# Kernel tuning notes

Hardware: AMD Instinct MI355X
Metric: run time of the kernel (lower is better)

## Reference

```python
import jax, jax.numpy as jnp
import numpy as np

B, S, D, H = 256, 64, 1024, 16
DH = D // H          # 64
BOARD = 8
NREL = 2 * (BOARD - 1) + 1  # 15


def _rel_indices():
    # Relative row/col offsets between all pairs of board squares, shifted to [0, 2*(BOARD-1)]
    coords = np.arange(S)
    row = coords // BOARD
    col = coords % BOARD
    rr = row[:, None] - row[None, :] + (BOARD - 1)  # (S, S)
    rc = col[:, None] - col[None, :] + (BOARD - 1)  # (S, S)
    return jnp.asarray(rr), jnp.asarray(rc)


def setup_inputs() -> dict:
    key = jax.random.key(0)
    ks = jax.random.split(key, 12)
    p = lambda k, sh: jax.random.normal(k, sh, jnp.float32) * 0.02
    return {
        "x": jax.random.normal(ks[0], (B, S, D), jnp.float32),
        "wq": p(ks[1], (D, D)),
        "wk": p(ks[2], (D, D)),
        "wv": p(ks[3], (D, D)),
        "wo": p(ks[4], (D, D)),
        "bo": jnp.zeros((D,), jnp.float32),
        "eq_h": p(ks[5], (NREL, DH)),
        "eq_w": p(ks[6], (NREL, DH)),
        "ek_h": p(ks[7], (NREL, DH)),
        "ek_w": p(ks[8], (NREL, DH)),
        "ev_h": p(ks[9], (NREL, DH)),
        "ev_w": p(ks[10], (NREL, DH)),
    }


def reference(x, wq, wk, wv, wo, bo, eq_h, eq_w, ek_h, ek_w, ev_h, ev_w):
    rr, rc = _rel_indices()
    rel_q = eq_h[rr] + eq_w[rc]  # (S, S, DH)
    rel_k = ek_h[rr] + ek_w[rc]
    rel_v = ev_h[rr] + ev_w[rc]

    def heads(y):
        return y.reshape(B, S, H, DH).transpose(0, 2, 1, 3)  # (B, H, S, DH)

    q = heads(x @ wq.T)
    k = heads(x @ wk.T)
    v = heads(x @ wv.T)

    # (q_i + rq_ij) . (k_j + rk_ij), expanded to avoid the (B,H,S,S,DH) intermediates
    scores = (
        jnp.einsum('bhid,bhjd->bhij', q, k)
        + jnp.einsum('bhid,ijd->bhij', q, rel_k)
        + jnp.einsum('ijd,bhjd->bhij', rel_q, k)
        + jnp.sum(rel_q * rel_k, axis=-1)[None, None]
    )
    attn = jax.nn.softmax(scores / jnp.sqrt(jnp.float32(DH)), axis=-1)  # (B, H, S, S)

    # sum_j attn_ij * (v_j + rv_ij)
    ctx = (
        jnp.einsum('bhij,bhjd->bhid', attn, v)
        + jnp.einsum('bhij,ijd->bhid', attn, rel_v)
    )
    ctx = ctx.transpose(0, 2, 1, 3).reshape(B, S, D)
    return ctx @ wo.T + bo
```

## Files before the change

kernel.cpp:

```cpp
#include <hip/hip_runtime.h>
#include <hip/hip_bf16.h>

typedef __hip_bfloat16 bf16;
typedef __attribute__((ext_vector_type(8))) short short8;
typedef __attribute__((ext_vector_type(8))) unsigned short ushort8;
typedef __attribute__((ext_vector_type(4))) float floatx4;

__device__ __forceinline__ short f2s(float x) {
  bf16 h = __float2bfloat16(x);
  short s;
  __builtin_memcpy(&s, &h, 2);
  return s;
}

__device__ __forceinline__ void gl_lds16(const bf16* g, bf16* l) {
  __builtin_amdgcn_global_load_lds(
      (const __attribute__((address_space(1))) unsigned int*)g,
      (__attribute__((address_space(3))) unsigned int*)l, 16, 0, 0);
}

#define MFMA16(a, b, c) __builtin_amdgcn_mfma_f32_16x16x32_bf16((a), (b), (c), 0, 0, 0)

__device__ __forceinline__ void bar() {
  asm volatile("" ::: "memory");
  __builtin_amdgcn_s_barrier();
  asm volatile("" ::: "memory");
}

#define VMCNT(N) asm volatile("s_waitcnt vmcnt(" #N ")" ::: "memory")

__global__ __launch_bounds__(256) void convert_f32_bf16(
    const float* __restrict__ src, bf16* __restrict__ dst, int n) {
  const int i = (blockIdx.x * 256 + threadIdx.x) * 8;
  if (i + 7 < n) {
    float4 a = *(const float4*)(src + i);
    float4 b = *(const float4*)(src + i + 4);
    short8 r;
    r[0] = f2s(a.x); r[1] = f2s(a.y); r[2] = f2s(a.z); r[3] = f2s(a.w);
    r[4] = f2s(b.x); r[5] = f2s(b.y); r[6] = f2s(b.z); r[7] = f2s(b.w);
    *(short8*)(dst + i) = r;
  }
}

__global__ __launch_bounds__(256) void precompute_tables(
    const float* __restrict__ eqh, const float* __restrict__ eqw,
    const float* __restrict__ ekh, const float* __restrict__ ekw,
    const float* __restrict__ evh, const float* __restrict__ evw,
    bf16* __restrict__ ews, float* __restrict__ S4f)
{
  const int t = threadIdx.x;
  if (t < 96) {
    const int tb = t >> 4, row = t & 15;
    const float* src[6] = {eqh, eqw, ekh, ekw, evh, evw};
    bf16* dst = ews + tb * 1024 + row * 64;
    if (row < 15) {
      const float* s = src[tb] + row * 64;
      #pragma unroll
      for (int d = 0; d < 64; d += 8) {
        float4 a = *(const float4*)(s + d);
        float4 b2 = *(const float4*)(s + d + 4);
        short8 rr;
        rr[0] = f2s(a.x); rr[1] = f2s(a.y); rr[2] = f2s(a.z); rr[3] = f2s(a.w);
        rr[4] = f2s(b2.x); rr[5] = f2s(b2.y); rr[6] = f2s(b2.z); rr[7] = f2s(b2.w);
        *(short8*)(dst + d) = rr;
      }
    } else {
      const short8 z = {0, 0, 0, 0, 0, 0, 0, 0};
      #pragma unroll
      for (int d = 0; d < 64; d += 8) *(short8*)(dst + d) = z;
    }
  }
  if (t < 225) {
    const int r = t / 15, c = t % 15;
    float s = 0.f;
    for (int d = 0; d < 64; ++d)
      s += (eqh[r * 64 + d] + eqw[c * 64 + d]) * (ekh[r * 64 + d] + ekw[c * 64 + d]);
    S4f[t] = s;
  }
}

template <int TAG>
__global__ __launch_bounds__(512, 2) void gemm256(
    const bf16* __restrict__ A,
    const bf16* __restrict__ W0, const bf16* __restrict__ W1, const bf16* __restrict__ W2,
    const float* __restrict__ bias, int hasBias,
    bf16* __restrict__ O0, bf16* __restrict__ O1, bf16* __restrict__ O2,
    float* __restrict__ Ofp, int outF32)
{
  __shared__ bf16 lds[65536];

  const int nx = gridDim.x;
  const int nwg = nx * gridDim.y;
  const int orig = blockIdx.y * nx + blockIdx.x;
  const int id = (orig & 7) * (nwg >> 3) + (orig >> 3);
  const int bx = id % nx;
  const int by = id / nx;

  const int m0 = bx * 256;
  const int which = by >> 2;
  const bf16* W = (which == 0) ? W0 : (which == 1) ? W1 : W2;
  bf16* O = (which == 0) ? O0 : (which == 1) ? O1 : O2;
  const int n0 = (by & 3) * 256;

  const int t = threadIdx.x;
  const int lane = t & 63, w = t >> 6;
  const int wm = w >> 2, wn = w & 3;
  const int quad = lane >> 4, n16 = lane & 15;

  const int srow = (t >> 6) * 16 + ((t & 63) >> 2);
  const int scol = ((t & 3) * 8) ^ (((t >> 5) & 1) << 4);
  const bf16* Abase = A + (m0 + srow) * 1024 + scol;
  const bf16* Bbase = W + (n0 + srow) * 1024 + scol;
  const int wdst = w * 512;

  const int swzq = (quad * 8) ^ ((n16 >> 3) << 4);
  const int aoff = wm * 4096 + n16 * 32 + swzq;
  const int boff = wn * 2048 + n16 * 32 + swzq;

  floatx4 acc[8][4];
  const floatx4 zero4 = {0.f, 0.f, 0.f, 0.f};
  #pragma unroll
  for (int mi = 0; mi < 8; ++mi)
    #pragma unroll
    for (int ni = 0; ni < 4; ++ni) acc[mi][ni] = zero4;

  #pragma unroll
  for (int p = 0; p < 3; ++p) {
    const bf16* ga = Abase + p * 32;
    bf16* la = lds + p * 16384 + wdst;
    gl_lds16(ga, la); gl_lds16(ga + 131072, la + 4096);
    const bf16* gb = Bbase + p * 32;
    bf16* lb = lds + p * 16384 + 8192 + wdst;
    gl_lds16(gb, lb); gl_lds16(gb + 131072, lb + 4096);
  }
  VMCNT(8);
  bar();

#define TILE_STEP(TT, DOSTAGE, WAITSEQ) do {                                   \
    const bf16* bA_ = lds + ((TT) & 3) * 16384;                                \
    const bf16* bB_ = bA_ + 8192;                                              \
    short8 af_[4], bq_[4];                                                     \
    _Pragma("unroll")                                                          \
    for (int mi = 0; mi < 4; ++mi)                                             \
      af_[mi] = *(const short8*)(bA_ + aoff + mi * 512);                       \
    _Pragma("unroll")                                                          \
    for (int ni = 0; ni < 4; ++ni)                                             \
      bq_[ni] = *(const short8*)(bB_ + boff + ni * 512);                       \
    if (DOSTAGE) {                                                             \
      const bf16* g_ = Abase + ((TT) + 3) * 32;                                \
      bf16* l_ = lds + (((TT) + 3) & 3) * 16384 + wdst;                        \
      gl_lds16(g_, l_); gl_lds16(g_ + 131072, l_ + 4096);                      \
    }                                                                          \
    bar();                                                                     \
    __builtin_amdgcn_s_setprio(1);                                             \
    _Pragma("unroll")                                                          \
    for (int mi = 0; mi < 4; ++mi)                                             \
      _Pragma("unroll")                                                        \
      for (int ni = 0; ni < 4; ++ni)                                           \
        acc[mi][ni] = MFMA16(af_[mi], bq_[ni], acc[mi][ni]);                   \
    __builtin_amdgcn_s_setprio(0);                                             \
    _Pragma("unroll")                                                          \
    for (int mi = 0; mi < 4; ++mi)                                             \
      af_[mi] = *(const short8*)(bA_ + aoff + 2048 + mi * 512);                \
    if (DOSTAGE) {                                                             \
      const bf16* g_ = Bbase + ((TT) + 3) * 32;                                \
      bf16* l_ = lds + (((TT) + 3) & 3) * 16384 + 8192 + wdst;                 \
      gl_lds16(g_, l_); gl_lds16(g_ + 131072, l_ + 4096);                      \
    }                                                                          \
    bar();                                                                     \
    __builtin_amdgcn_s_setprio(1);                                             \
    _Pragma("unroll")                                                          \
    for (int mi = 0; mi < 4; ++mi)                                             \
      _Pragma("unroll")                                                        \
      for (int ni = 0; ni < 4; ++ni)                                           \
        acc[mi + 4][ni] = MFMA16(af_[mi], bq_[ni], acc[mi + 4][ni]);           \
    __builtin_amdgcn_s_setprio(0);                                             \
    WAITSEQ;                                                                   \
  } while (0)

  #pragma unroll 1
  for (int tt = 0; tt < 29; ++tt) {
    TILE_STEP(tt, 1, VMCNT(8); bar());
  }
  TILE_STEP(29, 0, VMCNT(4); bar());
  TILE_STEP(30, 0, VMCNT(0); bar());
  TILE_STEP(31, 0, (void)0);
#undef TILE_STEP

  #pragma unroll
  for (int ni = 0; ni < 4; ++ni) {
    const int col = n0 + wn * 64 + ni * 16 + n16;
    const float bv = hasBias ? bias[col] : 0.f;
    #pragma unroll
    for (int mi = 0; mi < 8; ++mi) {
      #pragma unroll
      for (int r = 0; r < 4; ++r) {
        const int row = m0 + wm * 128 + mi * 16 + quad * 4 + r;
        if (outF32) Ofp[row * 1024 + col] = acc[mi][ni][r] + bv;
        else        O[row * 1024 + col] = __float2bfloat16(acc[mi][ni][r] + bv);
      }
    }
  }
}

template <int TAG>
__global__ __launch_bounds__(256) void gemm_bt(
    const bf16* __restrict__ A,
    const void* __restrict__ W0, const void* __restrict__ W1, const void* __restrict__ W2,
    int wBf,
    const float* __restrict__ bias, int hasBias,
    bf16* __restrict__ O0, bf16* __restrict__ O1, bf16* __restrict__ O2,
    float* __restrict__ Ofp, int outF32)
{
  __shared__ bf16 As[128 * 64];
  __shared__ bf16 Bs[128 * 64];

  const int m0 = blockIdx.x * 128;
  const int by = blockIdx.y;
  const int which = by >> 3;
  const void* W = (which == 0) ? W0 : (which == 1) ? W1 : W2;
  bf16* O = (which == 0) ? O0 : (which == 1) ? O1 : O2;
  const int n0 = (by & 7) * 128;

  const int t = threadIdx.x;
  const int lane = t & 63, w = t >> 6;
  const int lrow = lane >> 3, lcol = (lane & 7) * 8;
  const int wm = w >> 1, wn = w & 1;
  const int quad = lane >> 4, n16 = lane & 15;

  const int swzA = ((lrow & 1) << 5) | (((lrow >> 1) & 3) << 3);
  const int gcol = lcol ^ swzA;
  const int swzR = ((n16 & 1) << 5) | (((n16 >> 1) & 3) << 3);

  floatx4 acc[4][4];
  const floatx4 zero4 = {0.f, 0.f, 0.f, 0.f};
  #pragma unroll
  for (int mi = 0; mi < 4; ++mi)
    #pragma unroll
    for (int ni = 0; ni < 4; ++ni) acc[mi][ni] = zero4;

  const int arowb = m0 + w * 32 + lrow;
  const int browb = n0 + w * 32 + lrow;
  bf16* lau = As + w * 2048;
  bf16* lbu = Bs + w * 2048;

  if (wBf) {
    const bf16* Wb = (const bf16*)W;
    for (int k0 = 0; k0 < 1024; k0 += 64) {
      if (k0) __syncthreads();
      const bf16* ga = A + arowb * 1024 + k0 + gcol;
      const bf16* gw = Wb + browb * 1024 + k0 + gcol;
      #pragma unroll
      for (int c = 0; c < 4; ++c) {
        gl_lds16(ga + c * 8192, lau + c * 512);
        gl_lds16(gw + c * 8192, lbu + c * 512);
      }
      __syncthreads();
      #pragma unroll
      for (int ks = 0; ks < 2; ++ks) {
        short8 af[4], bfv[4];
        #pragma unroll
        for (int mi = 0; mi < 4; ++mi)
          af[mi] = *(const short8*)(As + (wm * 64 + mi * 16 + n16) * 64 +
                                    ((ks * 32 + quad * 8) ^ swzR));
        #pragma unroll
        for (int ni = 0; ni < 4; ++ni)
          bfv[ni] = *(const short8*)(Bs + (wn * 64 + ni * 16 + n16) * 64 +
                                     ((ks * 32 + quad * 8) ^ swzR));
        #pragma unroll
        for (int mi = 0; mi < 4; ++mi)
          #pragma unroll
          for (int ni = 0; ni < 4; ++ni)
            acc[mi][ni] = MFMA16(af[mi], bfv[ni], acc[mi][ni]);
      }
    }
  } else {
    const float* Wf = (const float*)W;
    for (int k0 = 0; k0 < 1024; k0 += 64) {
      short8 rb[4];
      #pragma unroll
      for (int c = 0; c < 4; ++c) {
        const float* f = Wf + (browb + c * 8) * 1024 + k0 + gcol;
        float4 a = *(const float4*)f;
        float4 b = *(const float4*)(f + 4);
        short8 r;
        r[0] = f2s(a.x); r[1] = f2s(a.y); r[2] = f2s(a.z); r[3] = f2s(a.w);
        r[4] = f2s(b.x); r[5] = f2s(b.y); r[6] = f2s(b.z); r[7] = f2s(b.w);
        rb[c] = r;
      }
      if (k0) __syncthreads();
      const bf16* ga = A + arowb * 1024 + k0 + gcol;
      #pragma unroll
      for (int c = 0; c < 4; ++c) {
        gl_lds16(ga + c * 8192, lau + c * 512);
        *(short8*)(lbu + lane * 8 + c * 512) = rb[c];
      }
      __syncthreads();
      #pragma unroll
      for (int ks = 0; ks < 2; ++ks) {
        short8 af[4], bfv[4];
        #pragma unroll
        for (int mi = 0; mi < 4; ++mi)
          af[mi] = *(const short8*)(As + (wm * 64 + mi * 16 + n16) * 64 +
                                    ((ks * 32 + quad * 8) ^ swzR));
        #pragma unroll
        for (int ni = 0; ni < 4; ++ni)
          bfv[ni] = *(const short8*)(Bs + (wn * 64 + ni * 16 + n16) * 64 +
                                     ((ks * 32 + quad * 8) ^ swzR));
        #pragma unroll
        for (int mi = 0; mi < 4; ++mi)
          #pragma unroll
          for (int ni = 0; ni < 4; ++ni)
            acc[mi][ni] = MFMA16(af[mi], bfv[ni], acc[mi][ni]);
      }
    }
  }

  #pragma unroll
  for (int ni = 0; ni < 4; ++ni) {
    const int col = n0 + wn * 64 + ni * 16 + n16;
    const float bv = hasBias ? bias[col] : 0.f;
    #pragma unroll
    for (int mi = 0; mi < 4; ++mi) {
      #pragma unroll
      for (int r = 0; r < 4; ++r) {
        const int row = m0 + wm * 64 + mi * 16 + quad * 4 + r;
        if (outF32) Ofp[row * 1024 + col] = acc[mi][ni][r] + bv;
        else        O[row * 1024 + col] = __float2bfloat16(acc[mi][ni][r] + bv);
      }
    }
  }
}

__global__ __launch_bounds__(256, 3) void attn_rel(
    const bf16* __restrict__ Q, const bf16* __restrict__ Km, const bf16* __restrict__ V,
    const bf16* __restrict__ ews, const float* __restrict__ S4f,
    bf16* __restrict__ Ctx)
{
  __shared__ bf16 vT[64][106];
  __shared__ bf16 pa[64][104];
  __shared__ float Ahs[64][16], Aws[64][16];
  __shared__ float Bhs[15][64], Bws[15][64];
  __shared__ float S4s[225];

  const int t = threadIdx.x;
  const int b = blockIdx.x >> 4, h = blockIdx.x & 15;
  const int base = b * 65536 + h * 64;
  const int lane = t & 63, w = t >> 6;
  const int quad = lane >> 4, n16 = lane & 15;

  const bf16* qrow = Q + base + (w * 16 + n16) * 1024 + quad * 8;
  short8 aq0 = *(const short8*)(qrow);
  short8 aq1 = *(const short8*)(qrow + 32);
  short8 bk0[4], bk1[4];
  #pragma unroll
  for (int nj = 0; nj < 4; ++nj) {
    const bf16* krow = Km + base + (nj * 16 + n16) * 1024 + quad * 8;
    bk0[nj] = *(const short8*)(krow);
    bk1[nj] = *(const short8*)(krow + 32);
  }
  short8 ebf[4][2];
  #pragma unroll
  for (int tb = 0; tb < 4; ++tb) {
    const bf16* er = ews + tb * 1024 + n16 * 64 + quad * 8;
    ebf[tb][0] = *(const short8*)(er);
    ebf[tb][1] = *(const short8*)(er + 32);
  }

  {
    const int r = t >> 2, c0 = (t & 3) * 16;
    const bf16* vrow = V + base + r * 1024 + c0;
    int4 v0 = *(const int4*)(vrow);
    int4 v1 = *(const int4*)(vrow + 8);
    const unsigned short* p0 = (const unsigned short*)&v0;
    const unsigned short* p1 = (const unsigned short*)&v1;
    #pragma unroll
    for (int ii = 0; ii < 8; ++ii) {
      *(unsigned short*)&vT[c0 + ii][r] = p0[ii];
      *(unsigned short*)&vT[c0 + 8 + ii][r] = p1[ii];
    }
    if (t < 60) {
      const int r2 = t >> 2, d0 = (t & 3) * 16;
      ushort8 pe0 = *(const ushort8*)(ews + 4096 + r2 * 64 + d0);
      ushort8 pe1 = *(const ushort8*)(ews + 4096 + r2 * 64 + d0 + 8);
      ushort8 pf0 = *(const ushort8*)(ews + 5120 + r2 * 64 + d0);
      ushort8 pf1 = *(const ushort8*)(ews + 5120 + r2 * 64 + d0 + 8);
      #pragma unroll
      for (int ii = 0; ii < 8; ++ii) {
        *(unsigned short*)&vT[d0 + ii][64 + r2] = pe0[ii];
        *(unsigned short*)&vT[d0 + 8 + ii][64 + r2] = pe1[ii];
        *(unsigned short*)&vT[d0 + ii][79 + r2] = pf0[ii];
        *(unsigned short*)&vT[d0 + 8 + ii][79 + r2] = pf1[ii];
      }
    }
    if (t < 64) {
      *(unsigned short*)&vT[t][94] = 0; *(unsigned short*)&vT[t][95] = 0;
      *(unsigned short*)&pa[t][94] = 0; *(unsigned short*)&pa[t][95] = 0;
    }
    if (t < 225) S4s[t] = S4f[t];
  }

  floatx4 cqk[4];
  #pragma unroll
  for (int nj = 0; nj < 4; ++nj) {
    floatx4 c = {0.f, 0.f, 0.f, 0.f};
    c = MFMA16(aq0, bk0[nj], c);
    c = MFMA16(aq1, bk1[nj], c);
    cqk[nj] = c;
  }
  {
    floatx4 cah = {0.f, 0.f, 0.f, 0.f}, caw = cah, cbh = cah, cbw = cah;
    cah = MFMA16(aq0, ebf[2][0], cah); cah = MFMA16(aq1, ebf[2][1], cah);
    caw = MFMA16(aq0, ebf[3][0], caw); caw = MFMA16(aq1, ebf[3][1], caw);
    cbh = MFMA16(bk0[w], ebf[0][0], cbh); cbh = MFMA16(bk1[w], ebf[0][1], cbh);
    cbw = MFMA16(bk0[w], ebf[1][0], cbw); cbw = MFMA16(bk1[w], ebf[1][1], cbw);
    #pragma unroll
    for (int r = 0; r < 4; ++r) {
      const int i = w * 16 + quad * 4 + r;
      Ahs[i][n16] = cah[r];
      Aws[i][n16] = caw[r];
      if (n16 < 15) { Bhs[n16][i] = cbh[r]; Bws[n16][i] = cbw[r]; }
    }
  }
  __syncthreads();

  const int i_base = w * 16 + quad * 4;
  float xv[4][4];
  #pragma unroll
  for (int nj = 0; nj < 4; ++nj) {
    const int j = nj * 16 + n16;
    const int rowj = j >> 3, colj = j & 7;
    #pragma unroll
    for (int r = 0; r < 4; ++r) {
      const int i = i_base + r;
      const int rowi = i >> 3, coli = i & 7;
      const int rr = rowi - rowj + 7, rc = coli - colj + 7;
      xv[r][nj] = (cqk[nj][r] + Ahs[i][rr] + Aws[i][rc] + Bhs[rr][j] + Bws[rc][j]
                   + S4s[rr * 15 + rc]) * 0.125f;
    }
  }
  #pragma unroll
  for (int r = 0; r < 4; ++r) {
    const int i = i_base + r;
    const int rowi = i >> 3, coli = i & 7;
    float mx = fmaxf(fmaxf(xv[r][0], xv[r][1]), fmaxf(xv[r][2], xv[r][3]));
    #pragma unroll
    for (int off = 1; off < 16; off <<= 1) mx = fmaxf(mx, __shfl_xor(mx, off));
    float p[4];
    float sm = 0.f;
    #pragma unroll
    for (int nj = 0; nj < 4; ++nj) { p[nj] = __expf(xv[r][nj] - mx); sm += p[nj]; }
    #pragma unroll
    for (int off = 1; off < 16; off <<= 1) sm += __shfl_xor(sm, off);
    const float inv = 1.0f / sm;
    #pragma unroll
    for (int nj = 0; nj < 4; ++nj) {
      p[nj] *= inv;
      pa[i][nj * 16 + n16] = __float2bfloat16(p[nj]);
    }
    float ph[4];
    #pragma unroll
    for (int nj = 0; nj < 4; ++nj) {
      float v = p[nj];
      v += __shfl_xor(v, 1); v += __shfl_xor(v, 2); v += __shfl_xor(v, 4);
      ph[nj] = v;
    }
    float s4 = p[0] + p[1] + p[2] + p[3];
    float pw = s4 + __shfl_xor(s4, 8);
    if ((n16 & 7) == 0) {
      const int hh = n16 >> 3;
      #pragma unroll
      for (int nj = 0; nj < 4; ++nj) {
        const int g = nj * 2 + hh;
        pa[i][64 + rowi + 7 - g] = __float2bfloat16(ph[nj]);
      }
    } else if (n16 < 8) {
      const int z = n16 - 1;
      pa[i][64 + (z < rowi ? z : z + 8)] = __float2bfloat16(0.f);
    }
    if (n16 < 8) {
      pa[i][79 + coli + 7 - n16] = __float2bfloat16(pw);
    } else {
      const int z = n16 - 8;
      pa[i][79 + (z < coli ? z : z + 8)] = __float2bfloat16(0.f);
    }
  }
  __threadfence_block();

  short8 ap[3];
  #pragma unroll
  for (int ksb = 0; ksb < 3; ++ksb)
    ap[ksb] = *(const short8*)&pa[w * 16 + n16][ksb * 32 + quad * 8];
  #pragma unroll
  for (int nj = 0; nj < 4; ++nj) {
    floatx4 c = {0.f, 0.f, 0.f, 0.f};
    #pragma unroll
    for (int ksb = 0; ksb < 3; ++ksb) {
      short8 bv = *(const short8*)&vT[nj * 16 + n16][ksb * 32 + quad * 8];
      c = MFMA16(ap[ksb], bv, c);
    }
    #pragma unroll
    for (int r = 0; r < 4; ++r) {
      const int i = i_base + r;
      Ctx[base + i * 1024 + nj * 16 + n16] = __float2bfloat16(c[r]);
    }
  }
}

extern "C" void kernel_launch(void* const* d_in, const int* in_sizes, int n_in,
                              void* d_out, int out_size, void* d_ws, size_t ws_size,
                              hipStream_t stream) {
  const float* x   = (const float*)d_in[0];
  const float* wq  = (const float*)d_in[1];
  const float* wk  = (const float*)d_in[2];
  const float* wv  = (const float*)d_in[3];
  const float* wo  = (const float*)d_in[4];
  const float* bo  = (const float*)d_in[5];
  const float* eqh = (const float*)d_in[6];
  const float* eqw = (const float*)d_in[7];
  const float* ekh = (const float*)d_in[8];
  const float* ekw = (const float*)d_in[9];
  const float* evh = (const float*)d_in[10];
  const float* evw = (const float*)d_in[11];
  float* outf = (float*)d_out;

  const size_t hdr = (ws_size - 16384) & ~(size_t)1023;
  bf16* ewsB = (bf16*)((char*)d_ws + hdr);
  float* S4f = (float*)((char*)d_ws + hdr + 12288);
  precompute_tables<<<1, 256, 0, stream>>>(eqh, eqw, ekh, ekw, evh, evw, ewsB, S4f);

  if (ws_size >= (size_t)73 * 1024 * 1024) {
    bf16* qb = (bf16*)d_ws;
    bf16* kb = qb + 16777216;
    bf16* wqb = kb + 16777216;
    bf16* wkb = wqb + 1048576;
    bf16* wvb = wkb + 1048576;
    bf16* wob = wvb + 1048576;
    bf16* xb = (bf16*)d_out;
    bf16* vb = (bf16*)((char*)d_out + 33554432);

    convert_f32_bf16<<<8192, 256, 0, stream>>>(x, xb, 16777216);
    convert_f32_bf16<<<512, 256, 0, stream>>>(wq, wqb, 1048576);
    convert_f32_bf16<<<512, 256, 0, stream>>>(wk, wkb, 1048576);
    convert_f32_bf16<<<512, 256, 0, stream>>>(wv, wvb, 1048576);
    convert_f32_bf16<<<512, 256, 0, stream>>>(wo, wob, 1048576);

    gemm256<0><<<dim3(64, 12), 512, 0, stream>>>(
        xb, wqb, wkb, wvb, nullptr, 0, qb, kb, vb, nullptr, 0);
    attn_rel<<<dim3(4096), 256, 0, stream>>>(qb, kb, vb, ewsB, S4f, qb);
    gemm256<1><<<dim3(64, 4), 512, 0, stream>>>(
        qb, wob, nullptr, nullptr, bo, 1, nullptr, nullptr, nullptr, outf, 1);
  } else {
    bf16* xb0 = (bf16*)((char*)d_out + 16777216);
    bf16* xb1 = (bf16*)((char*)d_out + 50331648);
    bf16* vQ2 = (bf16*)((char*)d_out + 33554432);
    bf16* qb = (bf16*)d_ws;
    bf16* kb = qb + 8388608;
    const int fastW = (ws_size >= (size_t)42 * 1024 * 1024) ? 1 : 0;
    bf16* wqb = kb + 8388608;
    bf16* wkb = wqb + 1048576;
    bf16* wvb = wkb + 1048576;
    bf16* wob = wvb + 1048576;

    convert_f32_bf16<<<4096, 256, 0, stream>>>(x, xb0, 8388608);
    convert_f32_bf16<<<4096, 256, 0, stream>>>(x + 8388608, xb1, 8388608);
    if (fastW) {
      convert_f32_bf16<<<512, 256, 0, stream>>>(wq, wqb, 1048576);
      convert_f32_bf16<<<512, 256, 0, stream>>>(wk, wkb, 1048576);
      convert_f32_bf16<<<512, 256, 0, stream>>>(wv, wvb, 1048576);
      convert_f32_bf16<<<512, 256, 0, stream>>>(wo, wob, 1048576);
    }

    for (int hh = 0; hh < 2; ++hh) {
      const bf16* xh = hh ? xb1 : xb0;
      if (fastW) {
        gemm256<0><<<dim3(32, 12), 512, 0, stream>>>(
            xh, wqb, wkb, wvb, nullptr, 0, qb, kb, vQ2, nullptr, 0);
      } else {
        gemm_bt<0><<<dim3(64, 24), 256, 0, stream>>>(
            xh, (const void*)wq, (const void*)wk, (const void*)wv,
            0, nullptr, 0, qb, kb, vQ2, nullptr, 0);
      }
      attn_rel<<<dim3(2048), 256, 0, stream>>>(qb, kb, vQ2, ewsB, S4f, qb);
      if (fastW) {
        gemm256<1><<<dim3(32, 4), 512, 0, stream>>>(
            qb, wob, nullptr, nullptr, bo, 1, nullptr, nullptr, nullptr,
            outf + (size_t)hh * 8388608, 1);
      } else {
        gemm_bt<1><<<dim3(64, 8), 256, 0, stream>>>(
            qb, (const void*)wo, nullptr, nullptr,
            0, bo, 1, nullptr, nullptr, nullptr,
            outf + (size_t)hh * 8388608, 1);
      }
    }
  }
}
```

Measured before the change: 394.2 us.

## Stage GEMM epilogue through LDS for coalesced stores and remap XCD tile order

The 256x256 GEMM epilogue now writes each warp's accumulator fragments into a padded per-warp LDS staging area, then reads them back as rows and issues 16-byte vector global stores instead of scattered 2- or 4-byte stores. The workgroup-to-tile mapping also changes so that each XCD gets a contiguous range of M tiles across the N tiles, aiming for better L2 reuse of A rows. The bf16 path drops the bias add, which is fine only if that path never has a bias. Staging relies on lgkmcnt waits only, with no barrier, which is valid only because each warp uses its own LDS region.

```diff
diff --git a/kernel.cpp b/kernel.cpp
--- a/kernel.cpp
+++ b/kernel.cpp
@@ -28,6 +28,7 @@
 }
 
 #define VMCNT(N) asm volatile("s_waitcnt vmcnt(" #N ")" ::: "memory")
+#define LGKM0()  asm volatile("s_waitcnt lgkmcnt(0)" ::: "memory")
 
 __global__ __launch_bounds__(256) void convert_f32_bf16(
     const float* __restrict__ src, bf16* __restrict__ dst, int n) {
@@ -90,11 +91,12 @@
   __shared__ bf16 lds[65536];
 
   const int nx = gridDim.x;
-  const int nwg = nx * gridDim.y;
   const int orig = blockIdx.y * nx + blockIdx.x;
-  const int id = (orig & 7) * (nwg >> 3) + (orig >> 3);
-  const int bx = id % nx;
-  const int by = id / nx;
+  const int xcd = orig & 7;
+  const int c = orig >> 3;
+  const int bxp = nx >> 3;
+  const int bx = xcd * bxp + (c % bxp);
+  const int by = c / bxp;
 
   const int m0 = bx * 256;
   const int which = by >> 2;
@@ -187,17 +189,44 @@
   TILE_STEP(31, 0, (void)0);
 #undef TILE_STEP
 
-  #pragma unroll
-  for (int ni = 0; ni < 4; ++ni) {
-    const int col = n0 + wn * 64 + ni * 16 + n16;
-    const float bv = hasBias ? bias[col] : 0.f;
-    #pragma unroll
+  bf16* stg = lds + w * 8192;
+  if (outF32) {
+    float* fst = (float*)stg;
+    float bvv[4];
+    #pragma unroll
+    for (int ni = 0; ni < 4; ++ni)
+      bvv[ni] = hasBias ? bias[n0 + wn * 64 + ni * 16 + n16] : 0.f;
+    #pragma unroll 1
     for (int mi = 0; mi < 8; ++mi) {
       #pragma unroll
-      for (int r = 0; r < 4; ++r) {
-        const int row = m0 + wm * 128 + mi * 16 + quad * 4 + r;
-        if (outF32) Ofp[row * 1024 + col] = acc[mi][ni][r] + bv;
-        else        O[row * 1024 + col] = __float2bfloat16(acc[mi][ni][r] + bv);
+      for (int ni = 0; ni < 4; ++ni)
+        #pragma unroll
+        for (int r = 0; r < 4; ++r)
+          fst[(quad * 4 + r) * 68 + ni * 16 + n16] = acc[mi][ni][r] + bvv[ni];
+      LGKM0();
+      #pragma unroll
+      for (int p = 0; p < 4; ++p) {
+        const int rr = p * 4 + (lane >> 4);
+        float4 vv = *(const float4*)(fst + rr * 68 + (lane & 15) * 4);
+        const int grow = m0 + wm * 128 + mi * 16 + rr;
+        *(float4*)(Ofp + grow * 1024 + n0 + wn * 64 + (lane & 15) * 4) = vv;
+      }
+    }
+  } else {
+    #pragma unroll 1
+    for (int mi = 0; mi < 8; ++mi) {
+      #pragma unroll
+      for (int ni = 0; ni < 4; ++ni)
+        #pragma unroll
+        for (int r = 0; r < 4; ++r)
+          stg[(quad * 4 + r) * 72 + ni * 16 + n16] = __float2bfloat16(acc[mi][ni][r]);
+      LGKM0();
+      #pragma unroll
+      for (int p = 0; p < 2; ++p) {
+        const int rr = p * 8 + (lane >> 3);
+        short8 vv = *(const short8*)(stg + rr * 72 + (lane & 7) * 8);
+        const int grow = m0 + wm * 128 + mi * 16 + rr;
+        *(short8*)(O + grow * 1024 + n0 + wn * 64 + (lane & 7) * 8) = vv;
       }
     }
   }
```

New measurement: 489.5 us. +24.2%, slower.
